# Performance work log

Measured on AMD Instinct MI355X. Metric: run time of the kernel, lower is better.

Reference implementation:

```python
import jax, jax.numpy as jnp
import numpy as np

N_NODES = 100000
N_EDGES = 1600000
IN_F, HID_F, OUT_F = 128, 128, 64


def setup_inputs() -> dict:
    key = jax.random.key(0)
    ks = jax.random.split(key, 10)
    x = jax.random.normal(ks[0], (N_NODES, IN_F), dtype=jnp.float32)
    adj_row = jax.random.randint(ks[1], (N_EDGES,), 0, N_NODES, dtype=jnp.int64)
    adj_col = jax.random.randint(ks[2], (N_EDGES,), 0, N_NODES, dtype=jnp.int64)
    adj_val = jax.random.uniform(ks[3], (N_EDGES,), dtype=jnp.float32)
    # layer weights (xavier-normal-ish scale), stored as [in, out]
    def w(k, fin, fout):
        return jax.random.normal(k, (fin, fout), dtype=jnp.float32) * jnp.sqrt(2.0 / (fin + fout))
    return {
        "x": x, "adj_row": adj_row, "adj_col": adj_col, "adj_val": adj_val,
        "W0": w(ks[4], IN_F, HID_F), "b0": jnp.zeros((HID_F,), jnp.float32),
        "W1": w(ks[5], HID_F, HID_F), "b1": jnp.zeros((HID_F,), jnp.float32),
        "W2": w(ks[6], HID_F, OUT_F), "b2": jnp.zeros((OUT_F,), jnp.float32),
    }


def _spmm(adj_row, adj_col, adj_val, h):
    # sparse [N,N] @ dense [N,F]: gather source rows, scale, scatter-add to dest
    msgs = adj_val[:, None] * h[adj_col]            # [E, F]
    return jax.ops.segment_sum(msgs, adj_row, num_segments=N_NODES)


def reference(x, adj_row, adj_col, adj_val, W0, b0, W1, b1, W2, b2):
    h = x
    params = [(W0, b0), (W1, b1), (W2, b2)]
    n_layers = len(params)
    for i, (W, b) in enumerate(params):
        h = h @ W + b                               # Linear
        h = _spmm(adj_row, adj_col, adj_val, h)     # torch.sparse.mm(adj, h)
        if i != n_layers - 1:
            h = jax.nn.relu(h)                      # activation on hidden layers only
    return h


if __name__ == "__main__":
    out = reference(**setup_inputs())
    print(out.shape)
```

## Files before the change

kernel.cpp:

```cpp
#include <hip/hip_runtime.h>
#include <hip/hip_bf16.h>

#define N_NODES 100000
#define N_EDGES 1600000

#define BIN_SHIFT 9
#define NBIN 196
#define NBLK 256
#define CHUNK 6250
#define SCAN_N (NBIN * NBLK)

typedef __attribute__((ext_vector_type(8))) short bf16x8;
typedef __attribute__((ext_vector_type(4))) float f32x4;

__device__ inline unsigned short f2bf(float f) {
    union { float f; unsigned u; } v; v.f = f;
    unsigned r = v.u + 0x7FFF + ((v.u >> 16) & 1);
    return (unsigned short)(r >> 16);
}
__device__ inline float bf2f(unsigned short h) {
    union { unsigned u; float f; } v; v.u = ((unsigned)h) << 16;
    return v.f;
}


__global__ __launch_bounds__(256) void p1_bincnt(const int* __restrict__ row,
                                                 int* __restrict__ cnt) {
    __shared__ int h[NBIN];
    for (int i = threadIdx.x; i < NBIN; i += 256) h[i] = 0;
    __syncthreads();
    int base = blockIdx.x * CHUNK;
    int end = base + CHUNK; if (end > N_EDGES) end = N_EDGES;
    for (int i = base + threadIdx.x; i < end; i += 256)
        atomicAdd(&h[row[i] >> BIN_SHIFT], 1);
    __syncthreads();
    for (int b = threadIdx.x; b < NBIN; b += 256)
        cnt[b * NBLK + blockIdx.x] = h[b];
}

__global__ __launch_bounds__(1024) void p2_scan(const int* __restrict__ cnt,
                                                int* __restrict__ base,
                                                int* __restrict__ rp) {
    __shared__ int s[1024];
    int t = threadIdx.x;
    const int per = SCAN_N / 1024;
    int lo = t * per, hi = lo + per;
    int sum = 0;
    for (int i = lo; i < hi; ++i) sum += cnt[i];
    s[t] = sum;
    __syncthreads();
    for (int off = 1; off < 1024; off <<= 1) {
        int v = (t >= off) ? s[t - off] : 0;
        __syncthreads();
        s[t] += v;
        __syncthreads();
    }
    int run = s[t] - sum;
    for (int i = lo; i < hi; ++i) { int c = cnt[i]; base[i] = run; run += c; }
    if (t == 0) rp[N_NODES] = N_EDGES;
}

__global__ __launch_bounds__(256) void p3_partition(const int* __restrict__ row,
                                                    const int* __restrict__ col,
                                                    const float* __restrict__ val,
                                                    const int* __restrict__ base,
                                                    int2* __restrict__ bout) {
    __shared__ int cur[NBIN];
    for (int i = threadIdx.x; i < NBIN; i += 256)
        cur[i] = base[i * NBLK + blockIdx.x];
    __syncthreads();
    int lo = blockIdx.x * CHUNK;
    int end = lo + CHUNK; if (end > N_EDGES) end = N_EDGES;
    for (int i = lo + threadIdx.x; i < end; i += 256) {
        int r = row[i];
        int b = r >> BIN_SHIFT;
        int p = atomicAdd(&cur[b], 1);
        int2 rec;
        rec.x = col[i] | ((r & 511) << 17);
        rec.y = __float_as_int(val[i]);
        bout[p] = rec;
    }
}

__global__ __launch_bounds__(256) void p4_binscatter(const int* __restrict__ base,
                                                     const int2* __restrict__ bin_in,
                                                     int* __restrict__ rp,
                                                     int2* __restrict__ erec) {
    __shared__ int cnt[512];
    __shared__ int part[256];
    const int b = blockIdx.x;
    const int t = threadIdx.x;
    const int lo = base[b * NBLK];
    const int hi = (b + 1 < NBIN) ? base[(b + 1) * NBLK] : N_EDGES;

    cnt[t] = 0; cnt[t + 256] = 0;
    __syncthreads();
    for (int e = lo + t; e < hi; e += 256)
        atomicAdd(&cnt[(unsigned)bin_in[e].x >> 17], 1);
    __syncthreads();

    int s0 = cnt[2 * t], s1 = cnt[2 * t + 1];
    int tsum = s0 + s1;
    part[t] = tsum;
    __syncthreads();
    for (int off = 1; off < 256; off <<= 1) {
        int v = (t >= off) ? part[t - off] : 0;
        __syncthreads();
        part[t] += v;
        __syncthreads();
    }
    int run = part[t] - tsum;
    cnt[2 * t] = run;
    cnt[2 * t + 1] = run + s0;

    const int rowbase = b << BIN_SHIFT;
    int r0 = rowbase + 2 * t, r1 = rowbase + 2 * t + 1;
    if (r0 < N_NODES) rp[r0] = lo + run;
    if (r1 < N_NODES) rp[r1] = lo + run + s0;
    __syncthreads();

    for (int e = lo + t; e < hi; e += 256) {
        int2 q = bin_in[e];
        int rl = (unsigned)q.x >> 17;
        int p = lo + atomicAdd(&cnt[rl], 1);
        int2 rec;
        rec.x = q.x & 0x1FFFF;
        rec.y = q.y;
        erec[p] = rec;
    }
}


__global__ __launch_bounds__(256) void pack_all(const float* __restrict__ W0,
                                                const float* __restrict__ W1,
                                                const float* __restrict__ W2,
                                                unsigned short* __restrict__ Bp0,
                                                unsigned short* __restrict__ Bp1,
                                                unsigned short* __restrict__ Bp2) {
    int idx = blockIdx.x * 256 + threadIdx.x;
    const float* W; unsigned short* Bp; int fout, li;
    if (idx < 16384)      { W = W0; Bp = Bp0; fout = 128; li = idx; }
    else if (idx < 32768) { W = W1; Bp = Bp1; fout = 128; li = idx - 16384; }
    else                  { W = W2; Bp = Bp2; fout = 64;  li = idx - 32768; }
    int j = li & 7, lane = (li >> 3) & 63, kb = (li >> 9) & 3, nt = li >> 11;
    int k = kb * 32 + (lane >> 4) * 8 + j;
    int col = nt * 16 + (lane & 15);
    Bp[li] = f2bf(W[k * fout + col]);
}


template<int FOUT, bool AF32>
__global__ __launch_bounds__(256) void gemm_mfma(const void* __restrict__ Xv,
                                                 const unsigned short* __restrict__ Bp,
                                                 const float* __restrict__ bias,
                                                 unsigned short* __restrict__ Y, int n) {
    const int wave = threadIdx.x >> 6;
    const int lane = threadIdx.x & 63;
    const int l15 = lane & 15, kg = lane >> 4;
    const int nbase = blockIdx.y * 64;
    const int rowTile = blockIdx.x * 128 + wave * 32;

    int r0 = rowTile + l15;      if (r0 >= n) r0 = n - 1;
    int r1 = rowTile + 16 + l15; if (r1 >= n) r1 = n - 1;

    bf16x8 a0[4], a1[4];
    if constexpr (AF32) {
        const float* x0 = (const float*)Xv + (size_t)r0 * 128 + kg * 8;
        const float* x1 = (const float*)Xv + (size_t)r1 * 128 + kg * 8;
        #pragma unroll
        for (int kb = 0; kb < 4; ++kb) {
            float4 u = *reinterpret_cast<const float4*>(x0 + kb * 32);
            float4 v = *reinterpret_cast<const float4*>(x0 + kb * 32 + 4);
            a0[kb] = (bf16x8){(short)f2bf(u.x), (short)f2bf(u.y), (short)f2bf(u.z), (short)f2bf(u.w),
                              (short)f2bf(v.x), (short)f2bf(v.y), (short)f2bf(v.z), (short)f2bf(v.w)};
            float4 p = *reinterpret_cast<const float4*>(x1 + kb * 32);
            float4 q = *reinterpret_cast<const float4*>(x1 + kb * 32 + 4);
            a1[kb] = (bf16x8){(short)f2bf(p.x), (short)f2bf(p.y), (short)f2bf(p.z), (short)f2bf(p.w),
                              (short)f2bf(q.x), (short)f2bf(q.y), (short)f2bf(q.z), (short)f2bf(q.w)};
        }
    } else {
        const bf16x8* x0 = reinterpret_cast<const bf16x8*>((const unsigned short*)Xv + (size_t)r0 * 128 + kg * 8);
        const bf16x8* x1 = reinterpret_cast<const bf16x8*>((const unsigned short*)Xv + (size_t)r1 * 128 + kg * 8);
        #pragma unroll
        for (int kb = 0; kb < 4; ++kb) { a0[kb] = x0[kb * 4]; a1[kb] = x1[kb * 4]; }
    }

    f32x4 c0[4], c1[4];
    #pragma unroll
    for (int t = 0; t < 4; ++t) {
        c0[t] = (f32x4){0.f, 0.f, 0.f, 0.f};
        c1[t] = (f32x4){0.f, 0.f, 0.f, 0.f};
    }

    const bf16x8* bpv = reinterpret_cast<const bf16x8*>(Bp);
    #pragma unroll
    for (int nt = 0; nt < 4; ++nt) {
        int ntAbs = (nbase >> 4) + nt;
        const bf16x8* bp = bpv + (size_t)(ntAbs * 4) * 64 + lane;
        #pragma unroll
        for (int kb = 0; kb < 4; ++kb) {
            bf16x8 b = bp[kb * 64];
            c0[nt] = __builtin_amdgcn_mfma_f32_16x16x32_bf16(a0[kb], b, c0[nt], 0, 0, 0);
            c1[nt] = __builtin_amdgcn_mfma_f32_16x16x32_bf16(a1[kb], b, c1[nt], 0, 0, 0);
        }
    }

    #pragma unroll
    for (int nt = 0; nt < 4; ++nt) {
        int col = nbase + nt * 16 + l15;
        float bv = bias[col];
        int rb = rowTile + kg * 4;
        #pragma unroll
        for (int j = 0; j < 4; ++j) {
            int ra = rb + j;
            if (ra < n) Y[(size_t)ra * FOUT + col] = f2bf(c0[nt][j] + bv);
            int rc = rb + 16 + j;
            if (rc < n) Y[(size_t)rc * FOUT + col] = f2bf(c1[nt][j] + bv);
        }
    }
}


__global__ __launch_bounds__(256) void spmm_mid(const int* __restrict__ rp,
                                                const int2* __restrict__ erec,
                                                const unsigned* __restrict__ G,
                                                unsigned* __restrict__ Y, int n) {
    int node = blockIdx.x * 4 + (threadIdx.x >> 6);
    if (node >= n) return;
    int lane = threadIdx.x & 63;
    int e0 = rp[node], e1 = rp[node + 1];
    float a0 = 0.f, a1 = 0.f;
    const unsigned* Gf = G + lane;
    while (e0 < e1) {
        int take = e1 - e0; if (take > 64) take = 64;
        int2 rec = erec[e0 + (lane < take ? lane : take - 1)];
        for (int i = 0; i < take; i += 16) {
            unsigned g[16]; float v[16];
            #pragma unroll
            for (int j = 0; j < 16; ++j) {
                int idx = i + j;
                bool ok = idx < take;
                idx = ok ? idx : take - 1;
                int c = __builtin_amdgcn_readlane(rec.x, idx);
                float vv = __int_as_float(__builtin_amdgcn_readlane(rec.y, idx));
                v[j] = ok ? vv : 0.f;
                g[j] = Gf[(size_t)c * 64];
            }
            __builtin_amdgcn_sched_barrier(0);
            #pragma unroll
            for (int j = 0; j < 16; ++j) {
                a0 += v[j] * bf2f((unsigned short)g[j]);
                a1 += v[j] * bf2f((unsigned short)(g[j] >> 16));
            }
        }
        e0 += take;
    }
    a0 = fmaxf(a0, 0.f); a1 = fmaxf(a1, 0.f);
    Y[(size_t)node * 64 + lane] = (unsigned)f2bf(a0) | ((unsigned)f2bf(a1) << 16);
}


__global__ __launch_bounds__(256) void spmm_last(const int* __restrict__ rp,
                                                 const int2* __restrict__ erec,
                                                 const unsigned short* __restrict__ G,
                                                 float* __restrict__ out, int n) {
    int node = blockIdx.x * 4 + (threadIdx.x >> 6);
    if (node >= n) return;
    int lane = threadIdx.x & 63;
    int e0 = rp[node], e1 = rp[node + 1];
    float acc = 0.f;
    const unsigned short* Gf = G + lane;
    while (e0 < e1) {
        int take = e1 - e0; if (take > 64) take = 64;
        int2 rec = erec[e0 + (lane < take ? lane : take - 1)];
        for (int i = 0; i < take; i += 16) {
            unsigned short g[16]; float v[16];
            #pragma unroll
            for (int j = 0; j < 16; ++j) {
                int idx = i + j;
                bool ok = idx < take;
                idx = ok ? idx : take - 1;
                int c = __builtin_amdgcn_readlane(rec.x, idx);
                float vv = __int_as_float(__builtin_amdgcn_readlane(rec.y, idx));
                v[j] = ok ? vv : 0.f;
                g[j] = Gf[(size_t)c * 64];
            }
            __builtin_amdgcn_sched_barrier(0);
            #pragma unroll
            for (int j = 0; j < 16; ++j)
                acc += v[j] * bf2f(g[j]);
        }
        e0 += take;
    }
    out[(size_t)node * 64 + lane] = acc;
}


extern "C" void kernel_launch(void* const* d_in, const int* in_sizes, int n_in,
                              void* d_out, int out_size, void* d_ws, size_t ws_size,
                              hipStream_t stream) {
    const float* x    = (const float*)d_in[0];
    const int*   arow = (const int*)d_in[1];
    const int*   acol = (const int*)d_in[2];
    const float* aval = (const float*)d_in[3];
    const float* W0   = (const float*)d_in[4];
    const float* b0   = (const float*)d_in[5];
    const float* W1   = (const float*)d_in[6];
    const float* b1   = (const float*)d_in[7];
    const float* W2   = (const float*)d_in[8];
    const float* b2   = (const float*)d_in[9];
    float* out = (float*)d_out;

    unsigned short* hlin = (unsigned short*)d_ws;
    unsigned short* hact = hlin + (size_t)N_NODES * 128;
    unsigned short* Bp0  = hact + (size_t)N_NODES * 128;
    unsigned short* Bp1  = Bp0 + 16384;
    unsigned short* Bp2  = Bp1 + 16384;
    int* cnt  = (int*)(Bp2 + 8192);
    int* base = cnt + SCAN_N;
    int* rp   = base + SCAN_N;
    int2* bin_in = (int2*)(rp + N_NODES + 2);
    int2* erec   = bin_in + N_EDGES;

    p1_bincnt<<<NBLK, 256, 0, stream>>>(arow, cnt);
    p2_scan<<<1, 1024, 0, stream>>>(cnt, base, rp);
    p3_partition<<<NBLK, 256, 0, stream>>>(arow, acol, aval, base, bin_in);
    p4_binscatter<<<NBIN, 256, 0, stream>>>(base, bin_in, rp, erec);

    pack_all<<<160, 256, 0, stream>>>(W0, W1, W2, Bp0, Bp1, Bp2);

    dim3 gemm_grid((N_NODES + 127) / 128, 2);
    dim3 gemm_grid2((N_NODES + 127) / 128, 1);
    int spmm_grid = (N_NODES + 3) / 4;

    gemm_mfma<128, true><<<gemm_grid, 256, 0, stream>>>(x, Bp0, b0, hlin, N_NODES);
    spmm_mid<<<spmm_grid, 256, 0, stream>>>(rp, erec, (const unsigned*)hlin, (unsigned*)hact, N_NODES);
    gemm_mfma<128, false><<<gemm_grid, 256, 0, stream>>>(hact, Bp1, b1, hlin, N_NODES);
    spmm_mid<<<spmm_grid, 256, 0, stream>>>(rp, erec, (const unsigned*)hlin, (unsigned*)hact, N_NODES);
    gemm_mfma<64, false><<<gemm_grid2, 256, 0, stream>>>(hact, Bp2, b2, hlin, N_NODES);
    spmm_last<<<spmm_grid, 256, 0, stream>>>(rp, erec, hlin, out, N_NODES);
}
```

Before: 321.4 us.

## Sort edges by column chunk within rows, vectorize last-layer SpMM gathers

The bin-scatter pass now sorts each row's edges by a coarse column bucket (col >> 14), using 4096 shared counters and a 16-way per-thread scan, so that gathers within a row touch nearby source rows for better cache locality. The mid-layer SpMM drops the masked 16-wide batch and sched barrier in favour of an 8-wide exact loop plus a scalar tail. The last-layer SpMM has each group of 8 lanes load 16-byte bf16 vectors for 8 edges at once and reduces across lanes with xor shuffles. This cuts the number of gather instructions but adds shuffle work, extra registers and more shared-memory pressure in the preprocessing kernel.

```diff
diff --git a/kernel.cpp b/kernel.cpp
--- a/kernel.cpp
+++ b/kernel.cpp
@@ -82,26 +82,32 @@
     }
 }
 
+
 __global__ __launch_bounds__(256) void p4_binscatter(const int* __restrict__ base,
                                                      const int2* __restrict__ bin_in,
                                                      int* __restrict__ rp,
                                                      int2* __restrict__ erec) {
-    __shared__ int cnt[512];
+    __shared__ int cnt[4096];
     __shared__ int part[256];
     const int b = blockIdx.x;
     const int t = threadIdx.x;
     const int lo = base[b * NBLK];
     const int hi = (b + 1 < NBIN) ? base[(b + 1) * NBLK] : N_EDGES;
 
-    cnt[t] = 0; cnt[t + 256] = 0;
-    __syncthreads();
-    for (int e = lo + t; e < hi; e += 256)
-        atomicAdd(&cnt[(unsigned)bin_in[e].x >> 17], 1);
-    __syncthreads();
-
-    int s0 = cnt[2 * t], s1 = cnt[2 * t + 1];
-    int tsum = s0 + s1;
-    part[t] = tsum;
+    for (int i = t; i < 4096; i += 256) cnt[i] = 0;
+    __syncthreads();
+    for (int e = lo + t; e < hi; e += 256) {
+        int2 q = bin_in[e];
+        int rl = (unsigned)q.x >> 17;
+        int ck = (q.x & 0x1FFFF) >> 14;
+        atomicAdd(&cnt[(rl << 3) | ck], 1);
+    }
+    __syncthreads();
+
+    int local[16]; int sum = 0;
+    #pragma unroll
+    for (int k = 0; k < 16; ++k) { local[k] = cnt[t * 16 + k]; sum += local[k]; }
+    part[t] = sum;
     __syncthreads();
     for (int off = 1; off < 256; off <<= 1) {
         int v = (t >= off) ? part[t - off] : 0;
@@ -109,22 +115,23 @@
         part[t] += v;
         __syncthreads();
     }
-    int run = part[t] - tsum;
-    cnt[2 * t] = run;
-    cnt[2 * t + 1] = run + s0;
+    int run = part[t] - sum;
+    #pragma unroll
+    for (int k = 0; k < 16; ++k) { int c = local[k]; cnt[t * 16 + k] = run; run += c; }
 
     const int rowbase = b << BIN_SHIFT;
     int r0 = rowbase + 2 * t, r1 = rowbase + 2 * t + 1;
-    if (r0 < N_NODES) rp[r0] = lo + run;
-    if (r1 < N_NODES) rp[r1] = lo + run + s0;
+    if (r0 < N_NODES) rp[r0] = lo + cnt[t * 16];
+    if (r1 < N_NODES) rp[r1] = lo + cnt[t * 16 + 8];
     __syncthreads();
 
     for (int e = lo + t; e < hi; e += 256) {
         int2 q = bin_in[e];
         int rl = (unsigned)q.x >> 17;
-        int p = lo + atomicAdd(&cnt[rl], 1);
+        int c = q.x & 0x1FFFF;
+        int p = lo + atomicAdd(&cnt[(rl << 3) | (c >> 14)], 1);
         int2 rec;
-        rec.x = q.x & 0x1FFFF;
+        rec.x = c;
         rec.y = q.y;
         erec[p] = rec;
     }
@@ -234,24 +241,27 @@
     while (e0 < e1) {
         int take = e1 - e0; if (take > 64) take = 64;
         int2 rec = erec[e0 + (lane < take ? lane : take - 1)];
-        for (int i = 0; i < take; i += 16) {
-            unsigned g[16]; float v[16];
+        int i = 0;
+        for (; i + 8 <= take; i += 8) {
+            unsigned g[8]; float v[8];
             #pragma unroll
-            for (int j = 0; j < 16; ++j) {
-                int idx = i + j;
-                bool ok = idx < take;
-                idx = ok ? idx : take - 1;
-                int c = __builtin_amdgcn_readlane(rec.x, idx);
-                float vv = __int_as_float(__builtin_amdgcn_readlane(rec.y, idx));
-                v[j] = ok ? vv : 0.f;
+            for (int j = 0; j < 8; ++j) {
+                int c = __builtin_amdgcn_readlane(rec.x, i + j);
+                v[j] = __int_as_float(__builtin_amdgcn_readlane(rec.y, i + j));
                 g[j] = Gf[(size_t)c * 64];
             }
-            __builtin_amdgcn_sched_barrier(0);
             #pragma unroll
-            for (int j = 0; j < 16; ++j) {
+            for (int j = 0; j < 8; ++j) {
                 a0 += v[j] * bf2f((unsigned short)g[j]);
                 a1 += v[j] * bf2f((unsigned short)(g[j] >> 16));
             }
+        }
+        for (; i < take; ++i) {
+            int c = __builtin_amdgcn_readlane(rec.x, i);
+            float v = __int_as_float(__builtin_amdgcn_readlane(rec.y, i));
+            unsigned g = Gf[(size_t)c * 64];
+            a0 += v * bf2f((unsigned short)g);
+            a1 += v * bf2f((unsigned short)(g >> 16));
         }
         e0 += take;
     }
@@ -267,32 +277,52 @@
     int node = blockIdx.x * 4 + (threadIdx.x >> 6);
     if (node >= n) return;
     int lane = threadIdx.x & 63;
+    int eg = lane >> 3, fg = lane & 7;
     int e0 = rp[node], e1 = rp[node + 1];
-    float acc = 0.f;
-    const unsigned short* Gf = G + lane;
+    float acc[8] = {0.f, 0.f, 0.f, 0.f, 0.f, 0.f, 0.f, 0.f};
     while (e0 < e1) {
         int take = e1 - e0; if (take > 64) take = 64;
         int2 rec = erec[e0 + (lane < take ? lane : take - 1)];
-        for (int i = 0; i < take; i += 16) {
-            unsigned short g[16]; float v[16];
+        for (int r = 0; r < take; r += 16) {
+            uint4 d[2]; float vv[2];
             #pragma unroll
-            for (int j = 0; j < 16; ++j) {
-                int idx = i + j;
+            for (int s = 0; s < 2; ++s) {
+                int idx = r + s * 8 + eg;
                 bool ok = idx < take;
-                idx = ok ? idx : take - 1;
-                int c = __builtin_amdgcn_readlane(rec.x, idx);
-                float vv = __int_as_float(__builtin_amdgcn_readlane(rec.y, idx));
-                v[j] = ok ? vv : 0.f;
-                g[j] = Gf[(size_t)c * 64];
+                int src = ok ? idx : take - 1;
+                int c = __shfl(rec.x, src);
+                float v = __int_as_float(__shfl(rec.y, src));
+                vv[s] = ok ? v : 0.f;
+                d[s] = *reinterpret_cast<const uint4*>(G + (size_t)c * 64 + fg * 8);
             }
-            __builtin_amdgcn_sched_barrier(0);
             #pragma unroll
-            for (int j = 0; j < 16; ++j)
-                acc += v[j] * bf2f(g[j]);
+            for (int s = 0; s < 2; ++s) {
+                unsigned w0 = d[s].x, w1 = d[s].y, w2 = d[s].z, w3 = d[s].w;
+                acc[0] += vv[s] * bf2f((unsigned short)w0);
+                acc[1] += vv[s] * bf2f((unsigned short)(w0 >> 16));
+                acc[2] += vv[s] * bf2f((unsigned short)w1);
+                acc[3] += vv[s] * bf2f((unsigned short)(w1 >> 16));
+                acc[4] += vv[s] * bf2f((unsigned short)w2);
+                acc[5] += vv[s] * bf2f((unsigned short)(w2 >> 16));
+                acc[6] += vv[s] * bf2f((unsigned short)w3);
+                acc[7] += vv[s] * bf2f((unsigned short)(w3 >> 16));
+            }
         }
         e0 += take;
     }
-    out[(size_t)node * 64 + lane] = acc;
+    #pragma unroll
+    for (int k = 0; k < 8; ++k) {
+        acc[k] += __shfl_xor(acc[k], 8);
+        acc[k] += __shfl_xor(acc[k], 16);
+        acc[k] += __shfl_xor(acc[k], 32);
+    }
+    if (eg == 0) {
+        float4 oA = {acc[0], acc[1], acc[2], acc[3]};
+        float4 oB = {acc[4], acc[5], acc[6], acc[7]};
+        float4* o = reinterpret_cast<float4*>(out + (size_t)node * 64 + fg * 8);
+        o[0] = oA;
+        o[1] = oB;
+    }
 }
 
 
```

Result: faster. 303.5 us (-5.5%).
